# Kernel tuning notes

Measured on AMD Instinct MI355X. Metric: run time of the kernel, lower is better.

## Reference

```python
import jax, jax.numpy as jnp
import numpy as np

H, D = 4, 32
C = H * D  # 128
EPS = 1e-5
N_NODES, N_EDGES = 80000, 1280000
IN_DIM = 45  # 22 static + 12 dynamic + 7 prog + 4 time
INV_SQRT_D = float(1.0 / np.sqrt(D))


def layer_norm(x, g, b):
    mu = jnp.mean(x, axis=-1, keepdims=True)
    var = jnp.mean((x - mu) ** 2, axis=-1, keepdims=True)
    return (x - mu) * jax.lax.rsqrt(var + EPS) * g + b


def transformer_conv(x, src, dst, Wq, bq, Wk, bk, Wv, bv, Ws, bs):
    # PyG TransformerConv (UniMP): query from dst node, key/value from src node,
    # segment softmax over incoming edges of each dst node, concat heads, + root skip.
    N = x.shape[0]
    q = (x @ Wq + bq).reshape(N, H, D)
    k = (x @ Wk + bk).reshape(N, H, D)
    v = (x @ Wv + bv).reshape(N, H, D)
    scores = jnp.sum(q[dst] * k[src], axis=-1) * INV_SQRT_D  # [E, H]
    m = jax.ops.segment_max(scores, dst, num_segments=N)     # [N, H]
    m = jnp.where(jnp.isfinite(m), m, 0.0)                   # nodes with no in-edges
    e = jnp.exp(scores - m[dst])
    denom = jax.ops.segment_sum(e, dst, num_segments=N)
    alpha = e / (denom[dst] + 1e-16)                          # [E, H]
    agg = jax.ops.segment_sum(alpha[..., None] * v[src], dst, num_segments=N)
    return agg.reshape(N, C) + x @ Ws + bs                    # root_weight skip


def gnn_block(x, src, dst, g, b, Wq, bq, Wk, bk, Wv, bv, Ws, bs):
    h = layer_norm(x, g, b)
    h = transformer_conv(h, src, dst, Wq, bq, Wk, bk, Wv, bv, Ws, bs)
    return x + jax.nn.relu(h)


def forward(x_static, x_dynamic, x_prog, x_time, edge_index, proj_w, ln_g, ln_b,
            Wq, bq, Wk, bk, Wv, bv, Ws, bs,
            fc1_w, fc1_b, fc2_w, fc2_b, fc3_w, fc3_b, fc4_w, fc4_b):
    src, dst = edge_index[0], edge_index[1]
    x = jnp.concatenate([x_static, x_dynamic, x_prog, x_time], axis=-1) @ proj_w
    blk = lambda t, l: gnn_block(t, src, dst, ln_g[l], ln_b[l], Wq[l], bq[l],
                                 Wk[l], bk[l], Wv[l], bv[l], Ws[l], bs[l])
    x = blk(x, 0)
    x = blk(x, 1)
    x_pi = blk(x, 2)  # dropout identity at inference
    x_dg = blk(x, 3)
    lrelu = lambda t: jax.nn.leaky_relu(t, 0.2)
    prog = lrelu(x_pi @ fc1_w + fc1_b) @ fc3_w + fc3_b  # [N, 7]
    diag = lrelu(x_dg @ fc2_w + fc2_b) @ fc4_w + fc4_b  # [N, 3]
    return prog, diag


def setup_inputs() -> dict:
    key = jax.random.key(0)
    ks = iter(jax.random.split(key, 32))
    nrm = lambda shape, s=0.05: jax.random.normal(next(ks), shape, dtype=jnp.float32) * s
    return {
        'x_static': jax.random.normal(next(ks), (N_NODES, 22), dtype=jnp.float32),
        'x_dynamic': jax.random.normal(next(ks), (N_NODES, 12), dtype=jnp.float32),
        'x_prog': jax.random.normal(next(ks), (N_NODES, 7), dtype=jnp.float32),
        'x_time': jax.random.normal(next(ks), (N_NODES, 4), dtype=jnp.float32),
        'edge_index': jax.random.randint(next(ks), (2, N_EDGES), 0, N_NODES, dtype=jnp.int32),
        'proj_w': nrm((IN_DIM, C), 0.1),
        'ln_g': jnp.ones((4, C), jnp.float32),
        'ln_b': jnp.zeros((4, C), jnp.float32),
        'Wq': nrm((4, C, C)), 'bq': jnp.zeros((4, C), jnp.float32),
        'Wk': nrm((4, C, C)), 'bk': jnp.zeros((4, C), jnp.float32),
        'Wv': nrm((4, C, C)), 'bv': jnp.zeros((4, C), jnp.float32),
        'Ws': nrm((4, C, C)), 'bs': jnp.zeros((4, C), jnp.float32),
        'fc1_w': nrm((C, C)), 'fc1_b': jnp.zeros((C,), jnp.float32),
        'fc2_w': nrm((C, C)), 'fc2_b': jnp.zeros((C,), jnp.float32),
        'fc3_w': nrm((C, 7)), 'fc3_b': jnp.zeros((7,), jnp.float32),
        'fc4_w': nrm((C, 3)), 'fc4_b': jnp.zeros((3,), jnp.float32),
    }


def reference(x_static, x_dynamic, x_prog, x_time, edge_index, proj_w, ln_g, ln_b,
              Wq, bq, Wk, bk, Wv, bv, Ws, bs,
              fc1_w, fc1_b, fc2_w, fc2_b, fc3_w, fc3_b, fc4_w, fc4_b):
    return forward(x_static, x_dynamic, x_prog, x_time, edge_index, proj_w, ln_g, ln_b,
                   Wq, bq, Wk, bk, Wv, bv, Ws, bs,
                   fc1_w, fc1_b, fc2_w, fc2_b, fc3_w, fc3_b, fc4_w, fc4_b)
```

## Files before the change

### kernel.cpp

```cpp
#include <hip/hip_runtime.h>
#include <hip/hip_bf16.h>
#include <cstdio>

#define INV_SQRT_D 0.17677669529663687f

typedef __attribute__((ext_vector_type(8))) short short8;
typedef __attribute__((ext_vector_type(4))) float f32x4;

static __device__ __forceinline__ unsigned short f2bf(float f) {
    __hip_bfloat16 h = __float2bfloat16(f);
    return *reinterpret_cast<unsigned short*>(&h);
}
static __device__ __forceinline__ float bf2f(unsigned short u) {
    return __uint_as_float(((unsigned)u) << 16);
}

__global__ __launch_bounds__(256) void proj_kernel(
    const float* __restrict__ xs, const float* __restrict__ xd,
    const float* __restrict__ xp, const float* __restrict__ xt,
    const float* __restrict__ W, float* __restrict__ x, int N)
{
    __shared__ float xsm[32][48];
    int t = threadIdx.x;
    int n0 = blockIdx.x * 32;
    for (int idx = t; idx < 32 * 45; idx += 256) {
        int row = idx / 45, c = idx - row * 45;
        int nrow = n0 + row;
        int nr = nrow < N ? nrow : N - 1;
        float v;
        if (c < 22)      v = xs[(size_t)nr * 22 + c];
        else if (c < 34) v = xd[(size_t)nr * 12 + (c - 22)];
        else if (c < 41) v = xp[(size_t)nr * 7 + (c - 34)];
        else             v = xt[(size_t)nr * 4 + (c - 41)];
        xsm[row][c] = v;
    }
    __syncthreads();

    int rg = t >> 6;
    int c0 = (t & 63) * 2;
    float acc0[8], acc1[8];
    #pragma unroll
    for (int i = 0; i < 8; ++i) { acc0[i] = 0.f; acc1[i] = 0.f; }
    for (int k = 0; k < 45; ++k) {
        float2 w = *(const float2*)(W + (size_t)k * 128 + c0);
        #pragma unroll
        for (int rr = 0; rr < 8; ++rr) {
            float xv = xsm[rg * 8 + rr][k];
            acc0[rr] += xv * w.x;
            acc1[rr] += xv * w.y;
        }
    }
    #pragma unroll
    for (int rr = 0; rr < 8; ++rr) {
        int row = n0 + rg * 8 + rr;
        if (row < N)
            *(float2*)&x[(size_t)row * 128 + c0] = make_float2(acc0[rr], acc1[rr]);
    }
}

__global__ __launch_bounds__(256) void deg_kernel(
    const int* __restrict__ dst, int* __restrict__ deg, int E)
{
    int e = blockIdx.x * 256 + threadIdx.x;
    if (e < E) atomicAdd(&deg[dst[e]], 1);
}

__global__ __launch_bounds__(256) void scan_reduce(
    const int* __restrict__ deg, int* __restrict__ blocksum, int n)
{
    int b = blockIdx.x, t = threadIdx.x;
    int idx = b * 1024 + t * 4;
    int s = 0;
    if (idx + 3 < n) {
        int4 v = *(const int4*)(deg + idx);
        s = v.x + v.y + v.z + v.w;
    } else if (idx < n) {
        s = deg[idx];
        if (idx + 1 < n) s += deg[idx + 1];
        if (idx + 2 < n) s += deg[idx + 2];
        if (idx + 3 < n) s += deg[idx + 3];
    }
    #pragma unroll
    for (int off = 1; off < 64; off <<= 1) s += __shfl_xor(s, off);
    __shared__ int ws[4];
    if ((t & 63) == 0) ws[t >> 6] = s;
    __syncthreads();
    if (t == 0) blocksum[b] = ws[0] + ws[1] + ws[2] + ws[3];
}

__global__ __launch_bounds__(1024) void scan_chunks(
    const int* __restrict__ blocksum, int* __restrict__ blockoff,
    int* __restrict__ row_start, int nb, int n)
{
    __shared__ int buf[2][1024];
    int t = threadIdx.x;
    int v = (t < nb) ? blocksum[t] : 0;
    int x = v;
    buf[0][t] = x;
    __syncthreads();
    int sel = 0;
    for (int off = 1; off < 1024; off <<= 1) {
        int y = (t >= off) ? buf[sel][t - off] : 0;
        x += y;
        buf[sel ^ 1][t] = x;
        sel ^= 1;
        __syncthreads();
    }
    if (t < nb) blockoff[t] = x - v;
    if (t == nb - 1) row_start[n] = x;
}

__global__ __launch_bounds__(256) void scan_write(
    const int* __restrict__ deg, const int* __restrict__ blockoff,
    int* __restrict__ row_start, int* __restrict__ cursor, int n)
{
    __shared__ int buf[2][256];
    int b = blockIdx.x, t = threadIdx.x;
    int idx = b * 1024 + t * 4;
    int v0 = 0, v1 = 0, v2 = 0, v3 = 0;
    if (idx + 3 < n) {
        int4 v = *(const int4*)(deg + idx);
        v0 = v.x; v1 = v.y; v2 = v.z; v3 = v.w;
    } else if (idx < n) {
        v0 = deg[idx];
        if (idx + 1 < n) v1 = deg[idx + 1];
        if (idx + 2 < n) v2 = deg[idx + 2];
        if (idx + 3 < n) v3 = deg[idx + 3];
    }
    int s = v0 + v1 + v2 + v3;
    int x = s;
    buf[0][t] = x;
    __syncthreads();
    int sel = 0;
    for (int off = 1; off < 256; off <<= 1) {
        int y = (t >= off) ? buf[sel][t - off] : 0;
        x += y;
        buf[sel ^ 1][t] = x;
        sel ^= 1;
        __syncthreads();
    }
    int ex = x - s + blockoff[b];
    if (idx < n)     { row_start[idx] = ex;     cursor[idx] = ex;     ex += v0; }
    if (idx + 1 < n) { row_start[idx + 1] = ex; cursor[idx + 1] = ex; ex += v1; }
    if (idx + 2 < n) { row_start[idx + 2] = ex; cursor[idx + 2] = ex; ex += v2; }
    if (idx + 3 < n) { row_start[idx + 3] = ex; cursor[idx + 3] = ex; }
}

__global__ __launch_bounds__(256) void scatter_kernel(
    const int* __restrict__ src, const int* __restrict__ dst,
    int* __restrict__ cursor, int* __restrict__ col_src, int E)
{
    int e = blockIdx.x * 256 + threadIdx.x;
    if (e < E) {
        int d = dst[e];
        int pos = atomicAdd(&cursor[d], 1);
        col_src[pos] = src[e];
    }
}

__global__ __launch_bounds__(256) void wcvt_kernel(
    const float* __restrict__ Wq, const float* __restrict__ Wk,
    const float* __restrict__ Wv, const float* __restrict__ Ws,
    unsigned short* __restrict__ Whi)
{
    __shared__ float lds[32][33];
    int b = blockIdx.x;
    int mat = b >> 4;
    int layer = mat >> 2, which = mat & 3;
    int tr = (b >> 2) & 3, tc = b & 3;
    int k0 = tr * 32, c0 = tc * 32;
    const float* Wsrc =
        (which == 0 ? Wq : which == 1 ? Wk : which == 2 ? Wv : Ws) +
        (size_t)layer * 16384;
    int t = threadIdx.x;
    #pragma unroll
    for (int i = 0; i < 4; ++i) {
        int kk = (t >> 5) + 8 * i, cc = t & 31;
        lds[kk][cc] = Wsrc[(size_t)(k0 + kk) * 128 + c0 + cc];
    }
    __syncthreads();
    #pragma unroll
    for (int i = 0; i < 4; ++i) {
        int cc = (t >> 5) + 8 * i, kk = t & 31;
        Whi[((size_t)mat * 128 + c0 + cc) * 128 + k0 + kk] = f2bf(lds[kk][cc]);
    }
}

__global__ __launch_bounds__(256) void lngemm_hs(
    const float* __restrict__ x, const float* __restrict__ g, const float* __restrict__ bb,
    const float* __restrict__ Ws, const float* __restrict__ bs,
    float* __restrict__ hs, int N)
{
    __shared__ float xsm[32][132];
    int t = threadIdx.x;
    int n0 = blockIdx.x * 32;
    {
        int r = t >> 3, cg = t & 7;
        int row = n0 + r;
        int rowc = row < N ? row : N - 1;
        const float* xr = x + (size_t)rowc * 128 + cg * 16;
        float4 u[4];
        #pragma unroll
        for (int i = 0; i < 4; ++i) u[i] = *(const float4*)(xr + i * 4);
        float s = 0.f, ss = 0.f;
        #pragma unroll
        for (int i = 0; i < 4; ++i) {
            s += u[i].x + u[i].y + u[i].z + u[i].w;
            ss += u[i].x * u[i].x + u[i].y * u[i].y + u[i].z * u[i].z + u[i].w * u[i].w;
        }
        s += __shfl_xor(s, 1); ss += __shfl_xor(ss, 1);
        s += __shfl_xor(s, 2); ss += __shfl_xor(ss, 2);
        s += __shfl_xor(s, 4); ss += __shfl_xor(ss, 4);
        float mu = s * (1.f / 128.f);
        float var = ss * (1.f / 128.f) - mu * mu;
        float rsv = rsqrtf(var + 1e-5f);
        const float* gp = g + cg * 16;
        const float* bp = bb + cg * 16;
        #pragma unroll
        for (int i = 0; i < 4; ++i) {
            float4 gv = *(const float4*)(gp + i * 4);
            float4 bv = *(const float4*)(bp + i * 4);
            float4 y;
            y.x = (u[i].x - mu) * rsv * gv.x + bv.x;
            y.y = (u[i].y - mu) * rsv * gv.y + bv.y;
            y.z = (u[i].z - mu) * rsv * gv.z + bv.z;
            y.w = (u[i].w - mu) * rsv * gv.w + bv.w;
            *(float4*)&xsm[r][cg * 16 + i * 4] = y;
        }
    }
    __syncthreads();

    int rg = t >> 6;
    int c0 = (t & 63) * 2;
    float acc0[8], acc1[8];
    #pragma unroll
    for (int i = 0; i < 8; ++i) { acc0[i] = 0.f; acc1[i] = 0.f; }
    for (int k = 0; k < 128; k += 4) {
        float2 w0 = *(const float2*)(Ws + (size_t)(k + 0) * 128 + c0);
        float2 w1 = *(const float2*)(Ws + (size_t)(k + 1) * 128 + c0);
        float2 w2 = *(const float2*)(Ws + (size_t)(k + 2) * 128 + c0);
        float2 w3 = *(const float2*)(Ws + (size_t)(k + 3) * 128 + c0);
        #pragma unroll
        for (int rr = 0; rr < 8; ++rr) {
            float4 xv = *(const float4*)&xsm[rg * 8 + rr][k];
            acc0[rr] += xv.x * w0.x + xv.y * w1.x + xv.z * w2.x + xv.w * w3.x;
            acc1[rr] += xv.x * w0.y + xv.y * w1.y + xv.z * w2.y + xv.w * w3.y;
        }
    }
    float b0 = bs[c0], b1 = bs[c0 + 1];
    #pragma unroll
    for (int rr = 0; rr < 8; ++rr) {
        int row = n0 + rg * 8 + rr;
        if (row < N) {
            float2 o = make_float2(acc0[rr] + b0, acc1[rr] + b1);
            *(float2*)&hs[(size_t)row * 128 + c0] = o;
        }
    }
}

__global__ __launch_bounds__(192) void qkv_mfma(
    const float* __restrict__ x, const float* __restrict__ g, const float* __restrict__ bb,
    const unsigned short* __restrict__ Wth,
    const float* __restrict__ bq, const float* __restrict__ bk, const float* __restrict__ bv,
    float* __restrict__ q, unsigned short* __restrict__ kvo, int N)
{
    __shared__ float lmu[16], lrs[16];
    int t = threadIdx.x;
    int n0 = blockIdx.x * 16;

    if (t < 128) {
        int r = t >> 3, cg = t & 7;
        int row = n0 + r;
        int rowc = row < N ? row : N - 1;
        const float* xr = x + (size_t)rowc * 128 + cg * 16;
        float s = 0.f, ss = 0.f;
        #pragma unroll
        for (int i = 0; i < 4; ++i) {
            float4 u = *(const float4*)(xr + i * 4);
            s += u.x + u.y + u.z + u.w;
            ss += u.x * u.x + u.y * u.y + u.z * u.z + u.w * u.w;
        }
        s += __shfl_xor(s, 1); ss += __shfl_xor(ss, 1);
        s += __shfl_xor(s, 2); ss += __shfl_xor(ss, 2);
        s += __shfl_xor(s, 4); ss += __shfl_xor(ss, 4);
        float mu = s * (1.f / 128.f);
        float var = ss * (1.f / 128.f) - mu * mu;
        float rsv = rsqrtf(var + 1e-5f);
        if (cg == 0) { lmu[r] = mu; lrs[r] = rsv; }
    }
    __syncthreads();

    int w = t >> 6;
    int l = t & 63;
    int lr = l & 15, lk = l >> 4;
    const unsigned short* Wh = Wth + (size_t)w * 16384;
    int arow = n0 + lr;
    int arowc = arow < N ? arow : (N - 1);
    float mu = lmu[lr], rsv = lrs[lr];

    f32x4 acc[8];
    #pragma unroll
    for (int n = 0; n < 8; ++n) acc[n] = (f32x4){0.f, 0.f, 0.f, 0.f};

    #pragma unroll
    for (int ks = 0; ks < 4; ++ks) {
        int k0 = ks * 32 + lk * 8;
        const float* xp = x + (size_t)arowc * 128 + k0;
        short8 ah;
        #pragma unroll
        for (int jj = 0; jj < 2; ++jj) {
            float4 xv = *(const float4*)(xp + jj * 4);
            float4 gv = *(const float4*)(g + k0 + jj * 4);
            float4 bv = *(const float4*)(bb + k0 + jj * 4);
            ah[jj * 4 + 0] = (short)f2bf((xv.x - mu) * rsv * gv.x + bv.x);
            ah[jj * 4 + 1] = (short)f2bf((xv.y - mu) * rsv * gv.y + bv.y);
            ah[jj * 4 + 2] = (short)f2bf((xv.z - mu) * rsv * gv.z + bv.z);
            ah[jj * 4 + 3] = (short)f2bf((xv.w - mu) * rsv * gv.w + bv.w);
        }
        #pragma unroll
        for (int n = 0; n < 8; ++n) {
            short8 bh = *(const short8*)(Wh + (size_t)(n * 16 + lr) * 128 + k0);
            acc[n] = __builtin_amdgcn_mfma_f32_16x16x32_bf16(ah, bh, acc[n], 0, 0, 0);
        }
    }

    const float* bias = (w == 0) ? bq : (w == 1) ? bk : bv;
    #pragma unroll
    for (int n = 0; n < 8; ++n) {
        int col = n * 16 + lr;
        float bsv = bias[col];
        #pragma unroll
        for (int j = 0; j < 4; ++j) {
            int orow = n0 + lk * 4 + j;
            if (orow < N) {
                float v = acc[n][j] + bsv;
                if (w == 0) q[(size_t)orow * 128 + col] = v;
                else if (w == 1) kvo[(size_t)orow * 256 + 2 * col] = f2bf(v);
                else kvo[(size_t)orow * 256 + 2 * col + 1] = f2bf(v);
            }
        }
    }
}

__global__ __launch_bounds__(256) void attn_kernel(
    const float* q, const unsigned short* __restrict__ kvp,
    const float* __restrict__ hs,
    const int* __restrict__ row_start, const int* __restrict__ col_src,
    const float* __restrict__ xin, float* xout, int N)
{
    int wid = threadIdx.x >> 6, lane = threadIdx.x & 63;
    int n = blockIdx.x * 4 + wid;
    if (n >= N) return;
    int c = lane * 2;
    float2 qv = *(const float2*)&q[(size_t)n * 128 + c];
    float qx = qv.x * INV_SQRT_D, qy = qv.y * INV_SQRT_D;
    int beg = row_start[n], end = row_start[n + 1];
    float den = 0.f, a0 = 0.f, a1 = 0.f;
    int i = beg;
    for (; i + 4 <= end; i += 4) {
        int s0 = col_src[i + 0];
        int s1 = col_src[i + 1];
        int s2 = col_src[i + 2];
        int s3 = col_src[i + 3];
        ushort4 kv0 = *(const ushort4*)(kvp + (size_t)s0 * 256 + 4 * lane);
        ushort4 kv1 = *(const ushort4*)(kvp + (size_t)s1 * 256 + 4 * lane);
        ushort4 kv2 = *(const ushort4*)(kvp + (size_t)s2 * 256 + 4 * lane);
        ushort4 kv3 = *(const ushort4*)(kvp + (size_t)s3 * 256 + 4 * lane);
        float p0 = qx * bf2f(kv0.x) + qy * bf2f(kv0.z);
        float p1 = qx * bf2f(kv1.x) + qy * bf2f(kv1.z);
        float p2 = qx * bf2f(kv2.x) + qy * bf2f(kv2.z);
        float p3 = qx * bf2f(kv3.x) + qy * bf2f(kv3.z);
        p0 += __shfl_xor(p0, 1); p1 += __shfl_xor(p1, 1);
        p2 += __shfl_xor(p2, 1); p3 += __shfl_xor(p3, 1);
        p0 += __shfl_xor(p0, 2); p1 += __shfl_xor(p1, 2);
        p2 += __shfl_xor(p2, 2); p3 += __shfl_xor(p3, 2);
        p0 += __shfl_xor(p0, 4); p1 += __shfl_xor(p1, 4);
        p2 += __shfl_xor(p2, 4); p3 += __shfl_xor(p3, 4);
        p0 += __shfl_xor(p0, 8); p1 += __shfl_xor(p1, 8);
        p2 += __shfl_xor(p2, 8); p3 += __shfl_xor(p3, 8);
        float w0 = __expf(p0), w1 = __expf(p1), w2 = __expf(p2), w3 = __expf(p3);
        den += (w0 + w1) + (w2 + w3);
        a0 += w0 * bf2f(kv0.y) + w1 * bf2f(kv1.y)
            + w2 * bf2f(kv2.y) + w3 * bf2f(kv3.y);
        a1 += w0 * bf2f(kv0.w) + w1 * bf2f(kv1.w)
            + w2 * bf2f(kv2.w) + w3 * bf2f(kv3.w);
    }
    for (; i < end; ++i) {
        int s = col_src[i];
        ushort4 kv = *(const ushort4*)(kvp + (size_t)s * 256 + 4 * lane);
        float p = qx * bf2f(kv.x) + qy * bf2f(kv.z);
        p += __shfl_xor(p, 1);
        p += __shfl_xor(p, 2);
        p += __shfl_xor(p, 4);
        p += __shfl_xor(p, 8);
        float w = __expf(p);
        den += w;
        a0 += w * bf2f(kv.y);
        a1 += w * bf2f(kv.w);
    }
    float inv = 1.f / (den + 1e-16f);
    float2 hv = *(const float2*)&hs[(size_t)n * 128 + c];
    float o0 = a0 * inv + hv.x;
    float o1 = a1 * inv + hv.y;
    o0 = o0 > 0.f ? o0 : 0.f;
    o1 = o1 > 0.f ? o1 : 0.f;
    float2 xv = *(const float2*)&xin[(size_t)n * 128 + c];
    xv.x += o0;
    xv.y += o1;
    *(float2*)&xout[(size_t)n * 128 + c] = xv;
}

__global__ __launch_bounds__(256) void head_kernel(
    const float* __restrict__ x, const float* __restrict__ fw,
    const float* __restrict__ fb, const float* __restrict__ ow,
    const float* __restrict__ ob, float* __restrict__ out, int OUTD, int N)
{
    __shared__ float xsm[32][132];
    __shared__ float tsm[32][132];
    int t = threadIdx.x;
    int n0 = blockIdx.x * 32;
    {
        int r = t >> 3, cg = t & 7;
        int row = n0 + r;
        int rowc = row < N ? row : N - 1;
        const float* xr = x + (size_t)rowc * 128 + cg * 16;
        #pragma unroll
        for (int i = 0; i < 4; ++i)
            *(float4*)&xsm[r][cg * 16 + i * 4] = *(const float4*)(xr + i * 4);
    }
    __syncthreads();

    int rg = t >> 6;
    int c0 = (t & 63) * 2;
    float acc0[8], acc1[8];
    #pragma unroll
    for (int i = 0; i < 8; ++i) { acc0[i] = 0.f; acc1[i] = 0.f; }
    for (int k = 0; k < 128; k += 4) {
        float2 w0 = *(const float2*)(fw + (size_t)(k + 0) * 128 + c0);
        float2 w1 = *(const float2*)(fw + (size_t)(k + 1) * 128 + c0);
        float2 w2 = *(const float2*)(fw + (size_t)(k + 2) * 128 + c0);
        float2 w3 = *(const float2*)(fw + (size_t)(k + 3) * 128 + c0);
        #pragma unroll
        for (int rr = 0; rr < 8; ++rr) {
            float4 xv = *(const float4*)&xsm[rg * 8 + rr][k];
            acc0[rr] += xv.x * w0.x + xv.y * w1.x + xv.z * w2.x + xv.w * w3.x;
            acc1[rr] += xv.x * w0.y + xv.y * w1.y + xv.z * w2.y + xv.w * w3.y;
        }
    }
    float b0 = fb[c0], b1 = fb[c0 + 1];
    #pragma unroll
    for (int rr = 0; rr < 8; ++rr) {
        float t0 = acc0[rr] + b0; t0 = (t0 > 0.f) ? t0 : 0.2f * t0;
        float t1 = acc1[rr] + b1; t1 = (t1 > 0.f) ? t1 : 0.2f * t1;
        tsm[rg * 8 + rr][c0] = t0;
        tsm[rg * 8 + rr][c0 + 1] = t1;
    }
    __syncthreads();

    int r2 = t >> 3, jo = t & 7;
    if (jo < OUTD) {
        float acc = 0.f;
        for (int k = 0; k < 128; k += 4) {
            float4 tv = *(const float4*)&tsm[r2][k];
            acc += tv.x * ow[(k + 0) * OUTD + jo];
            acc += tv.y * ow[(k + 1) * OUTD + jo];
            acc += tv.z * ow[(k + 2) * OUTD + jo];
            acc += tv.w * ow[(k + 3) * OUTD + jo];
        }
        int row = n0 + r2;
        if (row < N) out[(size_t)row * OUTD + jo] = acc + ob[jo];
    }
}

static inline size_t align_up(size_t v, size_t a) { return (v + a - 1) & ~(a - 1); }

extern "C" void kernel_launch(void* const* d_in, const int* in_sizes, int n_in,
                              void* d_out, int out_size, void* d_ws, size_t ws_size,
                              hipStream_t stream)
{
    const float* xs = (const float*)d_in[0];
    const float* xd = (const float*)d_in[1];
    const float* xp = (const float*)d_in[2];
    const float* xt = (const float*)d_in[3];
    const int* edge = (const int*)d_in[4];
    const float* proj_w = (const float*)d_in[5];
    const float* ln_g = (const float*)d_in[6];
    const float* ln_b = (const float*)d_in[7];
    const float* Wq = (const float*)d_in[8];
    const float* bq = (const float*)d_in[9];
    const float* Wk = (const float*)d_in[10];
    const float* bk = (const float*)d_in[11];
    const float* Wv = (const float*)d_in[12];
    const float* bv = (const float*)d_in[13];
    const float* Ws = (const float*)d_in[14];
    const float* bs = (const float*)d_in[15];
    const float* fc1_w = (const float*)d_in[16];
    const float* fc1_b = (const float*)d_in[17];
    const float* fc2_w = (const float*)d_in[18];
    const float* fc2_b = (const float*)d_in[19];
    const float* fc3_w = (const float*)d_in[20];
    const float* fc3_b = (const float*)d_in[21];
    const float* fc4_w = (const float*)d_in[22];
    const float* fc4_b = (const float*)d_in[23];

    int N = in_sizes[0] / 22;
    int E = in_sizes[4] / 2;
    const int* srcp = edge;
    const int* dstp = edge + E;

    char* w = (char*)d_ws;
    size_t off = 0;
    auto take = [&](size_t bytes) {
        char* p = w + off;
        off = align_up(off + bytes, 256);
        return p;
    };
    float* x = (float*)take((size_t)N * 128 * 4);
    float* q = (float*)take((size_t)N * 128 * 4);
    float* hsb = (float*)take((size_t)N * 128 * 4);
    unsigned short* kvb = (unsigned short*)take((size_t)N * 256 * 2);
    unsigned short* wth = (unsigned short*)take((size_t)16 * 128 * 128 * 2);
    int* deg = (int*)take((size_t)N * 4);
    int* row_start = (int*)take((size_t)(N + 1) * 4);
    int* cursor = (int*)take((size_t)N * 4);
    int* col_src = (int*)take((size_t)E * 4);
    int* blocksum = (int*)take((size_t)1024 * 4);
    int* blockoff = (int*)take((size_t)1024 * 4);
    if (off > ws_size) {
        fprintf(stderr, "kernel_launch: ws too small (%zu > %zu)\n", off, ws_size);
        return;
    }

    float* out = (float*)d_out;

    wcvt_kernel<<<256, 256, 0, stream>>>(Wq, Wk, Wv, Ws, wth);

    int nb = (N + 1023) >> 10;
    hipMemsetAsync(deg, 0, (size_t)N * 4, stream);
    deg_kernel<<<(E + 255) / 256, 256, 0, stream>>>(dstp, deg, E);
    scan_reduce<<<nb, 256, 0, stream>>>(deg, blocksum, N);
    scan_chunks<<<1, 1024, 0, stream>>>(blocksum, blockoff, row_start, nb, N);
    scan_write<<<nb, 256, 0, stream>>>(deg, blockoff, row_start, cursor, N);
    scatter_kernel<<<(E + 255) / 256, 256, 0, stream>>>(srcp, dstp, cursor, col_src, E);

    proj_kernel<<<(N + 31) / 32, 256, 0, stream>>>(
        xs, xd, xp, xt, proj_w, x, N);

    int hs_blocks = (N + 31) / 32;
    int qkv_blocks = (N + 15) / 16;
    int attn_blocks = (N + 3) / 4;
    int head_blocks = (N + 31) / 32;

    for (int l = 0; l < 4; ++l) {
        qkv_mfma<<<qkv_blocks, 192, 0, stream>>>(
            x, ln_g + l * 128, ln_b + l * 128, wth + (size_t)l * 65536,
            bq + l * 128, bk + l * 128, bv + l * 128, q, kvb, N);
        lngemm_hs<<<hs_blocks, 256, 0, stream>>>(
            x, ln_g + l * 128, ln_b + l * 128,
            Ws + (size_t)l * 16384, bs + l * 128, hsb, N);
        if (l == 2) {
            attn_kernel<<<attn_blocks, 256, 0, stream>>>(
                q, kvb, hsb, row_start, col_src, x, q, N);
            head_kernel<<<head_blocks, 256, 0, stream>>>(
                q, fc1_w, fc1_b, fc3_w, fc3_b, out, 7, N);
        } else {
            attn_kernel<<<attn_blocks, 256, 0, stream>>>(
                q, kvb, hsb, row_start, col_src, x, x, N);
        }
    }

    head_kernel<<<head_blocks, 256, 0, stream>>>(
        x, fc2_w, fc2_b, fc4_w, fc4_b, out + (size_t)N * 7, 3, N);
}
```

Before: 1.442 ms.

## Split wavefront across edges in attention and widen root-skip GEMM tiles

The attention kernel now has each wavefront process four edges at once: each 16-lane group handles one edge and every lane reads 16 bf16 k/v values with 128-bit loads. Per-edge shuffle reductions drop to two steps, and partial sums are combined across edge groups at the end. This gives more memory requests in flight per node and fewer shuffles, at the cost of more registers and masked work on nodes whose degree is not a multiple of 8. Separately, the root-skip GEMM kernel processes 64 rows per block with four output columns per thread, so weight loads are wider and reused across more rows.

```diff
diff --git a/kernel.cpp b/kernel.cpp
--- a/kernel.cpp
+++ b/kernel.cpp
@@ -5,6 +5,7 @@
 #define INV_SQRT_D 0.17677669529663687f
 
 typedef __attribute__((ext_vector_type(8))) short short8;
+typedef __attribute__((ext_vector_type(8))) unsigned short u16x8;
 typedef __attribute__((ext_vector_type(4))) float f32x4;
 
 static __device__ __forceinline__ unsigned short f2bf(float f) {
@@ -191,33 +192,32 @@
     const float* __restrict__ Ws, const float* __restrict__ bs,
     float* __restrict__ hs, int N)
 {
-    __shared__ float xsm[32][132];
+    __shared__ float xsm[64][132];
     int t = threadIdx.x;
-    int n0 = blockIdx.x * 32;
+    int n0 = blockIdx.x * 64;
     {
-        int r = t >> 3, cg = t & 7;
+        int r = t >> 2, cq = t & 3;
         int row = n0 + r;
         int rowc = row < N ? row : N - 1;
-        const float* xr = x + (size_t)rowc * 128 + cg * 16;
-        float4 u[4];
-        #pragma unroll
-        for (int i = 0; i < 4; ++i) u[i] = *(const float4*)(xr + i * 4);
+        const float* xr = x + (size_t)rowc * 128 + cq * 32;
+        float4 u[8];
+        #pragma unroll
+        for (int i = 0; i < 8; ++i) u[i] = *(const float4*)(xr + i * 4);
         float s = 0.f, ss = 0.f;
         #pragma unroll
-        for (int i = 0; i < 4; ++i) {
+        for (int i = 0; i < 8; ++i) {
             s += u[i].x + u[i].y + u[i].z + u[i].w;
             ss += u[i].x * u[i].x + u[i].y * u[i].y + u[i].z * u[i].z + u[i].w * u[i].w;
         }
         s += __shfl_xor(s, 1); ss += __shfl_xor(ss, 1);
         s += __shfl_xor(s, 2); ss += __shfl_xor(ss, 2);
-        s += __shfl_xor(s, 4); ss += __shfl_xor(ss, 4);
         float mu = s * (1.f / 128.f);
         float var = ss * (1.f / 128.f) - mu * mu;
         float rsv = rsqrtf(var + 1e-5f);
-        const float* gp = g + cg * 16;
-        const float* bp = bb + cg * 16;
-        #pragma unroll
-        for (int i = 0; i < 4; ++i) {
+        const float* gp = g + cq * 32;
+        const float* bp = bb + cq * 32;
+        #pragma unroll
+        for (int i = 0; i < 8; ++i) {
             float4 gv = *(const float4*)(gp + i * 4);
             float4 bv = *(const float4*)(bp + i * 4);
             float4 y;
@@ -225,35 +225,41 @@
             y.y = (u[i].y - mu) * rsv * gv.y + bv.y;
             y.z = (u[i].z - mu) * rsv * gv.z + bv.z;
             y.w = (u[i].w - mu) * rsv * gv.w + bv.w;
-            *(float4*)&xsm[r][cg * 16 + i * 4] = y;
-        }
-    }
-    __syncthreads();
-
-    int rg = t >> 6;
-    int c0 = (t & 63) * 2;
-    float acc0[8], acc1[8];
-    #pragma unroll
-    for (int i = 0; i < 8; ++i) { acc0[i] = 0.f; acc1[i] = 0.f; }
+            *(float4*)&xsm[r][cq * 32 + i * 4] = y;
+        }
+    }
+    __syncthreads();
+
+    int rg = t >> 5;
+    int c0 = (t & 31) * 4;
+    float4 acc[8];
+    #pragma unroll
+    for (int i = 0; i < 8; ++i) acc[i] = make_float4(0.f, 0.f, 0.f, 0.f);
     for (int k = 0; k < 128; k += 4) {
-        float2 w0 = *(const float2*)(Ws + (size_t)(k + 0) * 128 + c0);
-        float2 w1 = *(const float2*)(Ws + (size_t)(k + 1) * 128 + c0);
-        float2 w2 = *(const float2*)(Ws + (size_t)(k + 2) * 128 + c0);
-        float2 w3 = *(const float2*)(Ws + (size_t)(k + 3) * 128 + c0);
+        float4 w0 = *(const float4*)(Ws + (size_t)(k + 0) * 128 + c0);
+        float4 w1 = *(const float4*)(Ws + (size_t)(k + 1) * 128 + c0);
+        float4 w2 = *(const float4*)(Ws + (size_t)(k + 2) * 128 + c0);
+        float4 w3 = *(const float4*)(Ws + (size_t)(k + 3) * 128 + c0);
         #pragma unroll
         for (int rr = 0; rr < 8; ++rr) {
             float4 xv = *(const float4*)&xsm[rg * 8 + rr][k];
-            acc0[rr] += xv.x * w0.x + xv.y * w1.x + xv.z * w2.x + xv.w * w3.x;
-            acc1[rr] += xv.x * w0.y + xv.y * w1.y + xv.z * w2.y + xv.w * w3.y;
-        }
-    }
-    float b0 = bs[c0], b1 = bs[c0 + 1];
+            acc[rr].x += xv.x * w0.x + xv.y * w1.x + xv.z * w2.x + xv.w * w3.x;
+            acc[rr].y += xv.x * w0.y + xv.y * w1.y + xv.z * w2.y + xv.w * w3.y;
+            acc[rr].z += xv.x * w0.z + xv.y * w1.z + xv.z * w2.z + xv.w * w3.z;
+            acc[rr].w += xv.x * w0.w + xv.y * w1.w + xv.z * w2.w + xv.w * w3.w;
+        }
+    }
+    float4 bsv = *(const float4*)(bs + c0);
     #pragma unroll
     for (int rr = 0; rr < 8; ++rr) {
         int row = n0 + rg * 8 + rr;
         if (row < N) {
-            float2 o = make_float2(acc0[rr] + b0, acc1[rr] + b1);
-            *(float2*)&hs[(size_t)row * 128 + c0] = o;
+            float4 o;
+            o.x = acc[rr].x + bsv.x;
+            o.y = acc[rr].y + bsv.y;
+            o.z = acc[rr].z + bsv.z;
+            o.w = acc[rr].w + bsv.w;
+            *(float4*)&hs[(size_t)row * 128 + c0] = o;
         }
     }
 }
@@ -351,63 +357,87 @@
     int wid = threadIdx.x >> 6, lane = threadIdx.x & 63;
     int n = blockIdx.x * 4 + wid;
     if (n >= N) return;
-    int c = lane * 2;
-    float2 qv = *(const float2*)&q[(size_t)n * 128 + c];
-    float qx = qv.x * INV_SQRT_D, qy = qv.y * INV_SQRT_D;
+    int eg = lane >> 4;
+    int cg = lane & 15;
+    float qreg[8];
+    {
+        const float* qp = q + (size_t)n * 128 + cg * 8;
+        float4 q0 = *(const float4*)qp;
+        float4 q1 = *(const float4*)(qp + 4);
+        qreg[0] = q0.x * INV_SQRT_D; qreg[1] = q0.y * INV_SQRT_D;
+        qreg[2] = q0.z * INV_SQRT_D; qreg[3] = q0.w * INV_SQRT_D;
+        qreg[4] = q1.x * INV_SQRT_D; qreg[5] = q1.y * INV_SQRT_D;
+        qreg[6] = q1.z * INV_SQRT_D; qreg[7] = q1.w * INV_SQRT_D;
+    }
     int beg = row_start[n], end = row_start[n + 1];
-    float den = 0.f, a0 = 0.f, a1 = 0.f;
-    int i = beg;
-    for (; i + 4 <= end; i += 4) {
-        int s0 = col_src[i + 0];
-        int s1 = col_src[i + 1];
-        int s2 = col_src[i + 2];
-        int s3 = col_src[i + 3];
-        ushort4 kv0 = *(const ushort4*)(kvp + (size_t)s0 * 256 + 4 * lane);
-        ushort4 kv1 = *(const ushort4*)(kvp + (size_t)s1 * 256 + 4 * lane);
-        ushort4 kv2 = *(const ushort4*)(kvp + (size_t)s2 * 256 + 4 * lane);
-        ushort4 kv3 = *(const ushort4*)(kvp + (size_t)s3 * 256 + 4 * lane);
-        float p0 = qx * bf2f(kv0.x) + qy * bf2f(kv0.z);
-        float p1 = qx * bf2f(kv1.x) + qy * bf2f(kv1.z);
-        float p2 = qx * bf2f(kv2.x) + qy * bf2f(kv2.z);
-        float p3 = qx * bf2f(kv3.x) + qy * bf2f(kv3.z);
-        p0 += __shfl_xor(p0, 1); p1 += __shfl_xor(p1, 1);
-        p2 += __shfl_xor(p2, 1); p3 += __shfl_xor(p3, 1);
-        p0 += __shfl_xor(p0, 2); p1 += __shfl_xor(p1, 2);
-        p2 += __shfl_xor(p2, 2); p3 += __shfl_xor(p3, 2);
-        p0 += __shfl_xor(p0, 4); p1 += __shfl_xor(p1, 4);
-        p2 += __shfl_xor(p2, 4); p3 += __shfl_xor(p3, 4);
-        p0 += __shfl_xor(p0, 8); p1 += __shfl_xor(p1, 8);
-        p2 += __shfl_xor(p2, 8); p3 += __shfl_xor(p3, 8);
-        float w0 = __expf(p0), w1 = __expf(p1), w2 = __expf(p2), w3 = __expf(p3);
-        den += (w0 + w1) + (w2 + w3);
-        a0 += w0 * bf2f(kv0.y) + w1 * bf2f(kv1.y)
-            + w2 * bf2f(kv2.y) + w3 * bf2f(kv3.y);
-        a1 += w0 * bf2f(kv0.w) + w1 * bf2f(kv1.w)
-            + w2 * bf2f(kv2.w) + w3 * bf2f(kv3.w);
-    }
-    for (; i < end; ++i) {
-        int s = col_src[i];
-        ushort4 kv = *(const ushort4*)(kvp + (size_t)s * 256 + 4 * lane);
-        float p = qx * bf2f(kv.x) + qy * bf2f(kv.z);
-        p += __shfl_xor(p, 1);
-        p += __shfl_xor(p, 2);
-        p += __shfl_xor(p, 4);
-        p += __shfl_xor(p, 8);
-        float w = __expf(p);
-        den += w;
-        a0 += w * bf2f(kv.y);
-        a1 += w * bf2f(kv.w);
-    }
-    float inv = 1.f / (den + 1e-16f);
-    float2 hv = *(const float2*)&hs[(size_t)n * 128 + c];
-    float o0 = a0 * inv + hv.x;
-    float o1 = a1 * inv + hv.y;
-    o0 = o0 > 0.f ? o0 : 0.f;
-    o1 = o1 > 0.f ? o1 : 0.f;
-    float2 xv = *(const float2*)&xin[(size_t)n * 128 + c];
-    xv.x += o0;
-    xv.y += o1;
-    *(float2*)&xout[(size_t)n * 128 + c] = xv;
+    float den = 0.f;
+    float acc[8];
+    #pragma unroll
+    for (int j = 0; j < 8; ++j) acc[j] = 0.f;
+
+    for (int i = beg; i < end; i += 8) {
+        int e1 = i + eg, e2 = i + 4 + eg;
+        int s1 = col_src[e1 < end ? e1 : beg];
+        int s2 = col_src[e2 < end ? e2 : beg];
+        const unsigned short* r1 = kvp + (size_t)s1 * 256 + cg * 16;
+        const unsigned short* r2 = kvp + (size_t)s2 * 256 + cg * 16;
+        u16x8 a1 = *(const u16x8*)r1;
+        u16x8 b1 = *(const u16x8*)(r1 + 8);
+        u16x8 a2 = *(const u16x8*)r2;
+        u16x8 b2 = *(const u16x8*)(r2 + 8);
+        float p1 = qreg[0] * bf2f(a1[0]) + qreg[1] * bf2f(a1[2])
+                 + qreg[2] * bf2f(a1[4]) + qreg[3] * bf2f(a1[6])
+                 + qreg[4] * bf2f(b1[0]) + qreg[5] * bf2f(b1[2])
+                 + qreg[6] * bf2f(b1[4]) + qreg[7] * bf2f(b1[6]);
+        float p2 = qreg[0] * bf2f(a2[0]) + qreg[1] * bf2f(a2[2])
+                 + qreg[2] * bf2f(a2[4]) + qreg[3] * bf2f(a2[6])
+                 + qreg[4] * bf2f(b2[0]) + qreg[5] * bf2f(b2[2])
+                 + qreg[6] * bf2f(b2[4]) + qreg[7] * bf2f(b2[6]);
+        p1 += __shfl_xor(p1, 1); p2 += __shfl_xor(p2, 1);
+        p1 += __shfl_xor(p1, 2); p2 += __shfl_xor(p2, 2);
+        float w1 = (e1 < end) ? __expf(p1) : 0.f;
+        float w2 = (e2 < end) ? __expf(p2) : 0.f;
+        den += w1 + w2;
+        acc[0] += w1 * bf2f(a1[1]) + w2 * bf2f(a2[1]);
+        acc[1] += w1 * bf2f(a1[3]) + w2 * bf2f(a2[3]);
+        acc[2] += w1 * bf2f(a1[5]) + w2 * bf2f(a2[5]);
+        acc[3] += w1 * bf2f(a1[7]) + w2 * bf2f(a2[7]);
+        acc[4] += w1 * bf2f(b1[1]) + w2 * bf2f(b2[1]);
+        acc[5] += w1 * bf2f(b1[3]) + w2 * bf2f(b2[3]);
+        acc[6] += w1 * bf2f(b1[5]) + w2 * bf2f(b2[5]);
+        acc[7] += w1 * bf2f(b1[7]) + w2 * bf2f(b2[7]);
+    }
+
+    den += __shfl_xor(den, 16);
+    den += __shfl_xor(den, 32);
+    #pragma unroll
+    for (int j = 0; j < 8; ++j) {
+        acc[j] += __shfl_xor(acc[j], 16);
+        acc[j] += __shfl_xor(acc[j], 32);
+    }
+
+    if (eg == 0) {
+        float inv = 1.f / (den + 1e-16f);
+        const float* hp = hs + (size_t)n * 128 + cg * 8;
+        const float* xi = xin + (size_t)n * 128 + cg * 8;
+        float* xo = xout + (size_t)n * 128 + cg * 8;
+        float4 h0 = *(const float4*)hp;
+        float4 h1 = *(const float4*)(hp + 4);
+        float4 x0 = *(const float4*)xi;
+        float4 x1 = *(const float4*)(xi + 4);
+        float o;
+        float4 r0, r1;
+        o = acc[0] * inv + h0.x; r0.x = x0.x + (o > 0.f ? o : 0.f);
+        o = acc[1] * inv + h0.y; r0.y = x0.y + (o > 0.f ? o : 0.f);
+        o = acc[2] * inv + h0.z; r0.z = x0.z + (o > 0.f ? o : 0.f);
+        o = acc[3] * inv + h0.w; r0.w = x0.w + (o > 0.f ? o : 0.f);
+        o = acc[4] * inv + h1.x; r1.x = x1.x + (o > 0.f ? o : 0.f);
+        o = acc[5] * inv + h1.y; r1.y = x1.y + (o > 0.f ? o : 0.f);
+        o = acc[6] * inv + h1.z; r1.z = x1.z + (o > 0.f ? o : 0.f);
+        o = acc[7] * inv + h1.w; r1.w = x1.w + (o > 0.f ? o : 0.f);
+        *(float4*)xo = r0;
+        *(float4*)(xo + 4) = r1;
+    }
 }
 
 __global__ __launch_bounds__(256) void head_kernel(
@@ -546,7 +576,7 @@
     proj_kernel<<<(N + 31) / 32, 256, 0, stream>>>(
         xs, xd, xp, xt, proj_w, x, N);
 
-    int hs_blocks = (N + 31) / 32;
+    int hs_blocks = (N + 63) / 64;
     int qkv_blocks = (N + 15) / 16;
     int attn_blocks = (N + 3) / 4;
     int head_blocks = (N + 31) / 32;
```

Result: no change. 1.418 ms (-1.6%).
